# Optimization experiments

Measured on AMD Instinct MI355X. Metric: run time of the kernel, lower is better.

## Reference

```python
import jax, jax.numpy as jnp
import numpy as np

L, D_IN, D_HID, D_OUT, N = 8, 256, 1024, 256, 32768


def setup_inputs() -> dict:
    key = jax.random.key(0)
    kx, kp, kw1, kw2 = jax.random.split(key, 4)
    x = jax.random.normal(kx, (N, D_IN), dtype=jnp.float32)
    plane_idx = jax.random.randint(kp, (N,), 0, L, dtype=jnp.int32)
    W1 = jax.random.normal(kw1, (L, D_HID, D_IN), dtype=jnp.float32) * 0.014
    b1 = jnp.zeros((L, D_HID), dtype=jnp.float32)
    W2 = jax.random.normal(kw2, (L, D_OUT, D_HID), dtype=jnp.float32) * np.float32((2.0 / D_HID) ** 0.5)
    b2 = jnp.zeros((L, D_OUT), dtype=jnp.float32)
    return {"x": x, "W1": W1, "b1": b1, "W2": W2, "b2": b2, "plane_idx": plane_idx}


def reference(x, W1, b1, W2, b2, plane_idx):
    # Dense-dispatch MoE reference: scan over the L planes, run the full
    # 2-layer MLP for each plane's weights, and select per-walker rows via
    # the plane mask (equivalent math to gather -> MLP -> scatter).
    n_planes = W1.shape[0]
    out0 = jnp.zeros((x.shape[0], W2.shape[1]), dtype=x.dtype)

    def plane_step(out, p):
        h = jax.nn.gelu(x @ W1[p].T + b1[p], approximate=False)  # [N, D_hid]
        o = h @ W2[p].T + b2[p]                                  # [N, D_out]
        out = jnp.where((plane_idx == p)[:, None], o, out)
        return out, None

    out, _ = jax.lax.scan(plane_step, out0, jnp.arange(n_planes))
    return out
```

## Files before the change

### kernel.cpp

```cpp
#include <hip/hip_runtime.h>
#include <hip/hip_fp16.h>
#include <cstdint>

#define NT      32768
#define DIN     256
#define DHID    1024
#define DOUT    256
#define NPLANES 8
#define NBLK    (NT / 256)

typedef unsigned short u16;
typedef __attribute__((ext_vector_type(8))) _Float16 f16x8;
typedef __attribute__((ext_vector_type(4))) float    f32x4;

#define WS_OFFSETS 0
#define WS_META    64
#define WS_TP      1024
#define WS_TM      (WS_TP + 544*4)
#define WS_BLKHIST (WS_TM + 544*4)
#define WS_BLKBASE (WS_BLKHIST + NBLK*8*4)
#define WS_PERM    (WS_BLKBASE + NBLK*8*4)
#define WS_XB      (WS_PERM + NT*4)
#define WS_W1B     (WS_XB + NT*DIN*2)
#define WS_W2B     (WS_W1B + NPLANES*DHID*DIN*2)
#define WS_HB      (WS_W2B + NPLANES*DOUT*DHID*2)

__device__ __forceinline__ u16 f2h_bits(float f) {
    __half h = __float2half(f);
    return *reinterpret_cast<u16*>(&h);
}

__device__ __forceinline__ void gl_lds16(const void* g, void* l) {
    __builtin_amdgcn_global_load_lds(
        (const __attribute__((address_space(1))) void*)g,
        (__attribute__((address_space(3))) void*)l,
        16, 0, 0);
}

__global__ void prep_k(const int* __restrict__ pidx, const float* __restrict__ x,
                       const float* __restrict__ W1, const float* __restrict__ W2,
                       int* __restrict__ blkhist, u16* __restrict__ xb,
                       u16* __restrict__ w1b, u16* __restrict__ w2b) {
    __shared__ int cnt[NPLANES];
    const int t = threadIdx.x, lane = t & 63;
    if ((int)blockIdx.x < NBLK) {
        if (t < NPLANES) cnt[t] = 0;
        __syncthreads();
        const int p = pidx[blockIdx.x * 256 + t];
#pragma unroll
        for (int q = 0; q < NPLANES; ++q) {
            unsigned long long m = __ballot(p == q);
            if (p == q && __popcll(m & ((1ULL << lane) - 1)) == 0)
                atomicAdd(&cnt[q], __popcll(m));
        }
        __syncthreads();
        if (t < NPLANES) blkhist[blockIdx.x * NPLANES + t] = cnt[t];
    }
    const int n0 = NT * DIN / 4, n1 = NPLANES * DHID * DIN / 4, n2 = NPLANES * DOUT * DHID / 4;
    const int stride = gridDim.x * blockDim.x;
    for (int i = blockIdx.x * blockDim.x + t; i < n0 + n1 + n2; i += stride) {
        const float4* s; ushort4* d; int j;
        if (i < n0)           { s = (const float4*)x;  d = (ushort4*)xb;  j = i; }
        else if (i < n0 + n1) { s = (const float4*)W1; d = (ushort4*)w1b; j = i - n0; }
        else                  { s = (const float4*)W2; d = (ushort4*)w2b; j = i - n0 - n1; }
        float4 v = s[j];
        ushort4 o;
        o.x = f2h_bits(v.x); o.y = f2h_bits(v.y);
        o.z = f2h_bits(v.z); o.w = f2h_bits(v.w);
        d[j] = o;
    }
}

__global__ void scan_k(const int* __restrict__ blkhist, int* __restrict__ offsets,
                       int* __restrict__ blkbase, int* __restrict__ meta,
                       int* __restrict__ tp, int* __restrict__ tm) {
    __shared__ int tot[NPLANES];
    const int t = threadIdx.x;
    if (t < NPLANES) {
        int s = 0;
#pragma unroll 8
        for (int b = 0; b < NBLK; ++b) s += blkhist[b * NPLANES + t];
        tot[t] = s;
    }
    __syncthreads();
    if (t == 0) {
        int off = 0, tc = 0;
        for (int p = 0; p < NPLANES; ++p) {
            offsets[p] = off;
            for (int m = 0; m < tot[p]; m += 64) { tp[tc] = p; tm[tc] = m; ++tc; }
            off += tot[p];
        }
        offsets[NPLANES] = off;
        meta[0] = tc;
    }
    __syncthreads();
    if (t < NPLANES) {
        int run = offsets[t];
#pragma unroll 8
        for (int b = 0; b < NBLK; ++b) {
            blkbase[b * NPLANES + t] = run;
            run += blkhist[b * NPLANES + t];
        }
    }
}

__global__ void scatter_k(const int* __restrict__ pidx, const int* __restrict__ blkbase,
                          int* __restrict__ perm) {
    __shared__ int wcnt[4][NPLANES];
    __shared__ int wbase[4][NPLANES];
    const int t = threadIdx.x, lane = t & 63, wave = t >> 6;
    const int i = blockIdx.x * 256 + t;
    const int p = pidx[i];
    int rank = 0;
#pragma unroll
    for (int q = 0; q < NPLANES; ++q) {
        unsigned long long m = __ballot(p == q);
        if (lane == 0) wcnt[wave][q] = __popcll(m);
        if (p == q) rank = __popcll(m & ((1ULL << lane) - 1));
    }
    __syncthreads();
    if (t < NPLANES) {
        int run = blkbase[blockIdx.x * NPLANES + t];
#pragma unroll
        for (int w = 0; w < 4; ++w) { wbase[w][t] = run; run += wcnt[w][t]; }
    }
    __syncthreads();
    perm[wbase[wave][p] + rank] = i;
}

#define XCD_MAP(NSPLIT)                                                        \
    const int ntiles = meta[0];                                                \
    const int xcd = blockIdx.x & 7, idx = blockIdx.x >> 3;                     \
    const int q8 = ntiles >> 3, r8 = ntiles & 7;                               \
    const int tn = q8 + (xcd < r8 ? 1 : 0);                                    \
    if (idx >= tn * (NSPLIT)) return;                                          \
    const int tile = (xcd < r8 ? xcd * (q8 + 1)                                \
                               : r8 * (q8 + 1) + (xcd - r8) * q8)              \
                     + idx / (NSPLIT);                                         \
    const int n0v = (idx % (NSPLIT)) * 128;

__global__ __launch_bounds__(256, 4) void gemm1_k(
    const u16* __restrict__ xb, const u16* __restrict__ w1b,
    const float* __restrict__ b1, const int* __restrict__ perm,
    const int* __restrict__ offsets, const int* __restrict__ meta,
    const int* __restrict__ tp, const int* __restrict__ tm,
    u16* __restrict__ hb)
{
    __shared__ __align__(16) u16 smem[12288];
    XCD_MAP(8)
    const int p   = tp[tile];
    const int m0  = tm[tile];
    const int off = offsets[p];
    const int cnt = offsets[p + 1] - off;

    u16* const sA = smem;
    u16* const sB = smem + 4096;

    const int tid = threadIdx.x;
    const u16* aptr[2];
    const u16* bptr[4];
#pragma unroll
    for (int c = 0; c < 2; ++c) {
        const int slot = c * 256 + tid, row = slot >> 3, ch = slot & 7;
        const int gr = min(m0 + row, cnt - 1);
        aptr[c] = xb + (size_t)perm[off + gr] * DIN + ((ch ^ (row & 7)) * 8);
    }
#pragma unroll
    for (int c = 0; c < 4; ++c) {
        const int slot = c * 256 + tid, row = slot >> 3, ch = slot & 7;
        bptr[c] = w1b + ((size_t)p * DHID + n0v + row) * DIN + ((ch ^ (row & 7)) * 8);
    }
    const int wave = tid >> 6, lane = tid & 63;
    const int wr = wave >> 1, wc = wave & 1;
    const int lm = lane & 15, lk = lane >> 4;

    f32x4 acc[2][4];
#pragma unroll
    for (int a = 0; a < 2; ++a)
#pragma unroll
        for (int b = 0; b < 4; ++b) acc[a][b] = (f32x4){0.f, 0.f, 0.f, 0.f};

    for (int kt = 0; kt < DIN / 64; ++kt) {
        const int k0 = kt * 64;
#pragma unroll
        for (int c = 0; c < 2; ++c) gl_lds16(aptr[c] + k0, sA + c * 2048 + tid * 8);
#pragma unroll
        for (int c = 0; c < 4; ++c) gl_lds16(bptr[c] + k0, sB + c * 2048 + tid * 8);
        __syncthreads();
#pragma unroll
        for (int kk = 0; kk < 2; ++kk) {
            f16x8 af[2], bf[4];
#pragma unroll
            for (int mf = 0; mf < 2; ++mf) {
                const int row = wr * 32 + mf * 16 + lm;
                const int g   = kk * 4 + lk;
                af[mf] = *(const f16x8*)(sA + row * 64 + ((g ^ (row & 7)) * 8));
            }
#pragma unroll
            for (int nf = 0; nf < 4; ++nf) {
                const int row = wc * 64 + nf * 16 + lm;
                const int g   = kk * 4 + lk;
                bf[nf] = *(const f16x8*)(sB + row * 64 + ((g ^ (row & 7)) * 8));
            }
#pragma unroll
            for (int mf = 0; mf < 2; ++mf)
#pragma unroll
                for (int nf = 0; nf < 4; ++nf)
                    acc[mf][nf] = __builtin_amdgcn_mfma_f32_16x16x32_f16(
                        af[mf], bf[nf], acc[mf][nf], 0, 0, 0);
        }
        __syncthreads();
    }

    u16* const sOut = smem;
#pragma unroll
    for (int nf = 0; nf < 4; ++nf) {
        const int col = wc * 64 + nf * 16 + lm;
        const float bb = b1[p * DHID + n0v + col];
        const int cc = col >> 3, c7 = col & 7;
#pragma unroll
        for (int mf = 0; mf < 2; ++mf) {
#pragma unroll
            for (int j = 0; j < 4; ++j) {
                const int tok = wr * 32 + mf * 16 + lk * 4 + j;
                float v = acc[mf][nf][j] + bb;
                float g = 0.5f * v * (1.0f + erff(v * 0.70710678118654752f));
                sOut[tok * 128 + ((cc ^ (tok & 15)) * 8) + c7] = f2h_bits(g);
            }
        }
    }
    __syncthreads();
    const int r = tid >> 2, qq = tid & 3;
    if (m0 + r < cnt) {
        u16* dst = hb + (size_t)(off + m0 + r) * DHID + n0v;
#pragma unroll
        for (int c = 0; c < 4; ++c) {
            const int l = qq * 4 + c;
            *(int4*)(dst + l * 8) = *(const int4*)(sOut + r * 128 + ((l ^ (r & 15)) * 8));
        }
    }
}

__global__ __launch_bounds__(256, 4) void gemm2_k(
    const u16* __restrict__ hb, const u16* __restrict__ w2b,
    const float* __restrict__ b2, const int* __restrict__ perm,
    const int* __restrict__ offsets, const int* __restrict__ meta,
    const int* __restrict__ tp, const int* __restrict__ tm,
    float* __restrict__ out)
{
    __shared__ __align__(16) u16 smem[12288];
    XCD_MAP(2)
    const int p   = tp[tile];
    const int m0  = tm[tile];
    const int off = offsets[p];
    const int cnt = offsets[p + 1] - off;

    u16* const sA = smem;
    u16* const sB = smem + 4096;

    const int tid = threadIdx.x;
    const u16* aptr[2];
    const u16* bptr[4];
#pragma unroll
    for (int c = 0; c < 2; ++c) {
        const int slot = c * 256 + tid, row = slot >> 3, ch = slot & 7;
        aptr[c] = hb + (size_t)(off + min(m0 + row, cnt - 1)) * DHID + ((ch ^ (row & 7)) * 8);
    }
#pragma unroll
    for (int c = 0; c < 4; ++c) {
        const int slot = c * 256 + tid, row = slot >> 3, ch = slot & 7;
        bptr[c] = w2b + ((size_t)p * DOUT + n0v + row) * DHID + ((ch ^ (row & 7)) * 8);
    }
    const int wave = tid >> 6, lane = tid & 63;
    const int wr = wave >> 1, wc = wave & 1;
    const int lm = lane & 15, lk = lane >> 4;

    f32x4 acc[2][4];
#pragma unroll
    for (int a = 0; a < 2; ++a)
#pragma unroll
        for (int b = 0; b < 4; ++b) acc[a][b] = (f32x4){0.f, 0.f, 0.f, 0.f};

    for (int kt = 0; kt < DHID / 64; ++kt) {
        const int k0 = kt * 64;
#pragma unroll
        for (int c = 0; c < 2; ++c) gl_lds16(aptr[c] + k0, sA + c * 2048 + tid * 8);
#pragma unroll
        for (int c = 0; c < 4; ++c) gl_lds16(bptr[c] + k0, sB + c * 2048 + tid * 8);
        __syncthreads();
#pragma unroll
        for (int kk = 0; kk < 2; ++kk) {
            f16x8 af[2], bf[4];
#pragma unroll
            for (int mf = 0; mf < 2; ++mf) {
                const int row = wr * 32 + mf * 16 + lm;
                const int g   = kk * 4 + lk;
                af[mf] = *(const f16x8*)(sA + row * 64 + ((g ^ (row & 7)) * 8));
            }
#pragma unroll
            for (int nf = 0; nf < 4; ++nf) {
                const int row = wc * 64 + nf * 16 + lm;
                const int g   = kk * 4 + lk;
                bf[nf] = *(const f16x8*)(sB + row * 64 + ((g ^ (row & 7)) * 8));
            }
#pragma unroll
            for (int mf = 0; mf < 2; ++mf)
#pragma unroll
                for (int nf = 0; nf < 4; ++nf)
                    acc[mf][nf] = __builtin_amdgcn_mfma_f32_16x16x32_f16(
                        af[mf], bf[nf], acc[mf][nf], 0, 0, 0);
        }
        __syncthreads();
    }

#pragma unroll
    for (int nf = 0; nf < 4; ++nf) {
        const int col = n0v + wc * 64 + nf * 16 + lm;
        const float bb = b2[p * DOUT + col];
#pragma unroll
        for (int mf = 0; mf < 2; ++mf) {
#pragma unroll
            for (int j = 0; j < 4; ++j) {
                const int tok = wr * 32 + mf * 16 + lk * 4 + j;
                if (m0 + tok < cnt)
                    out[(size_t)perm[off + m0 + tok] * DOUT + col] = acc[mf][nf][j] + bb;
            }
        }
    }
}

extern "C" void kernel_launch(void* const* d_in, const int* in_sizes, int n_in,
                              void* d_out, int out_size, void* d_ws, size_t ws_size,
                              hipStream_t stream) {
    const float* x    = (const float*)d_in[0];
    const float* W1   = (const float*)d_in[1];
    const float* b1   = (const float*)d_in[2];
    const float* W2   = (const float*)d_in[3];
    const float* b2   = (const float*)d_in[4];
    const int*   pidx = (const int*)d_in[5];
    float*       out  = (float*)d_out;

    char* ws      = (char*)d_ws;
    int* offsets  = (int*)(ws + WS_OFFSETS);
    int* meta     = (int*)(ws + WS_META);
    int* tp       = (int*)(ws + WS_TP);
    int* tm       = (int*)(ws + WS_TM);
    int* blkhist  = (int*)(ws + WS_BLKHIST);
    int* blkbase  = (int*)(ws + WS_BLKBASE);
    int* perm     = (int*)(ws + WS_PERM);
    u16* xb       = (u16*)(ws + WS_XB);
    u16* w1b      = (u16*)(ws + WS_W1B);
    u16* w2b      = (u16*)(ws + WS_W2B);
    u16* hb       = (u16*)(ws + WS_HB);

    prep_k<<<2048, 256, 0, stream>>>(pidx, x, W1, W2, blkhist, xb, w1b, w2b);
    scan_k<<<1, 64, 0, stream>>>(blkhist, offsets, blkbase, meta, tp, tm);
    scatter_k<<<NBLK, 256, 0, stream>>>(pidx, blkbase, perm);

    gemm1_k<<<4224, 256, 0, stream>>>(xb, w1b, b1, perm, offsets, meta, tp, tm, hb);
    gemm2_k<<<1056, 256, 0, stream>>>(hb, w2b, b2, perm, offsets, meta, tp, tm, out);
}
```

Measured before the change: 115.5 us.

## Enlarge gemm1 token tile to 128 rows and use sigmoid-form GELU approximation

gemm1 now processes 128-token tiles with 512 threads, so each loaded W1 slice is reused across twice as many tokens. The scan kernel builds separate tile lists for gemm1 (128-row) and gemm2 (64-row), and the launch grids change to match. The exact erf GELU is replaced with a tanh-style approximation computed as x*sigmoid, using a fast exp and a reciprocal, to cut the cost of the epilogue. The approximation adds a small numerical deviation from the exact GELU. The aggressive launch bounds may also limit registers per thread and cause spills.

```diff
diff --git a/kernel.cpp b/kernel.cpp
--- a/kernel.cpp
+++ b/kernel.cpp
@@ -15,9 +15,11 @@
 
 #define WS_OFFSETS 0
 #define WS_META    64
-#define WS_TP      1024
-#define WS_TM      (WS_TP + 544*4)
-#define WS_BLKHIST (WS_TM + 544*4)
+#define WS_T1P     1024
+#define WS_T1M     (WS_T1P + 272*4)
+#define WS_T2P     (WS_T1M + 272*4)
+#define WS_T2M     (WS_T2P + 544*4)
+#define WS_BLKHIST (WS_T2M + 544*4)
 #define WS_BLKBASE (WS_BLKHIST + NBLK*8*4)
 #define WS_PERM    (WS_BLKBASE + NBLK*8*4)
 #define WS_XB      (WS_PERM + NT*4)
@@ -35,6 +37,12 @@
         (const __attribute__((address_space(1))) void*)g,
         (__attribute__((address_space(3))) void*)l,
         16, 0, 0);
+}
+
+__device__ __forceinline__ float gelu_fast(float x) {
+    const float u = x * (1.5957691216f + 0.07135481283f * x * x);
+    const float e = __expf(-u);
+    return x * __builtin_amdgcn_rcpf(1.0f + e);
 }
 
 __global__ void prep_k(const int* __restrict__ pidx, const float* __restrict__ x,
@@ -73,7 +81,8 @@
 
 __global__ void scan_k(const int* __restrict__ blkhist, int* __restrict__ offsets,
                        int* __restrict__ blkbase, int* __restrict__ meta,
-                       int* __restrict__ tp, int* __restrict__ tm) {
+                       int* __restrict__ t1p, int* __restrict__ t1m,
+                       int* __restrict__ t2p, int* __restrict__ t2m) {
     __shared__ int tot[NPLANES];
     const int t = threadIdx.x;
     if (t < NPLANES) {
@@ -84,14 +93,15 @@
     }
     __syncthreads();
     if (t == 0) {
-        int off = 0, tc = 0;
+        int off = 0, tc1 = 0, tc2 = 0;
         for (int p = 0; p < NPLANES; ++p) {
             offsets[p] = off;
-            for (int m = 0; m < tot[p]; m += 64) { tp[tc] = p; tm[tc] = m; ++tc; }
+            for (int m = 0; m < tot[p]; m += 128) { t1p[tc1] = p; t1m[tc1] = m; ++tc1; }
+            for (int m = 0; m < tot[p]; m += 64)  { t2p[tc2] = p; t2m[tc2] = m; ++tc2; }
             off += tot[p];
         }
         offsets[NPLANES] = off;
-        meta[0] = tc;
+        meta[0] = tc1; meta[1] = tc2;
     }
     __syncthreads();
     if (t < NPLANES) {
@@ -128,8 +138,8 @@
     perm[wbase[wave][p] + rank] = i;
 }
 
-#define XCD_MAP(NSPLIT)                                                        \
-    const int ntiles = meta[0];                                                \
+#define XCD_MAP(NSPLIT, NTILES)                                                \
+    const int ntiles = (NTILES);                                               \
     const int xcd = blockIdx.x & 7, idx = blockIdx.x >> 3;                     \
     const int q8 = ntiles >> 3, r8 = ntiles & 7;                               \
     const int tn = q8 + (xcd < r8 ? 1 : 0);                                    \
@@ -139,35 +149,31 @@
                      + idx / (NSPLIT);                                         \
     const int n0v = (idx % (NSPLIT)) * 128;
 
-__global__ __launch_bounds__(256, 4) void gemm1_k(
+__global__ __launch_bounds__(512, 8) void gemm1_k(
     const u16* __restrict__ xb, const u16* __restrict__ w1b,
     const float* __restrict__ b1, const int* __restrict__ perm,
     const int* __restrict__ offsets, const int* __restrict__ meta,
     const int* __restrict__ tp, const int* __restrict__ tm,
     u16* __restrict__ hb)
 {
-    __shared__ __align__(16) u16 smem[12288];
-    XCD_MAP(8)
+    __shared__ __align__(16) u16 smem[16384];
+    XCD_MAP(8, meta[0])
     const int p   = tp[tile];
     const int m0  = tm[tile];
     const int off = offsets[p];
     const int cnt = offsets[p + 1] - off;
 
     u16* const sA = smem;
-    u16* const sB = smem + 4096;
+    u16* const sB = smem + 8192;
 
     const int tid = threadIdx.x;
     const u16* aptr[2];
-    const u16* bptr[4];
+    const u16* bptr[2];
 #pragma unroll
     for (int c = 0; c < 2; ++c) {
-        const int slot = c * 256 + tid, row = slot >> 3, ch = slot & 7;
+        const int slot = c * 512 + tid, row = slot >> 3, ch = slot & 7;
         const int gr = min(m0 + row, cnt - 1);
         aptr[c] = xb + (size_t)perm[off + gr] * DIN + ((ch ^ (row & 7)) * 8);
-    }
-#pragma unroll
-    for (int c = 0; c < 4; ++c) {
-        const int slot = c * 256 + tid, row = slot >> 3, ch = slot & 7;
         bptr[c] = w1b + ((size_t)p * DHID + n0v + row) * DIN + ((ch ^ (row & 7)) * 8);
     }
     const int wave = tid >> 6, lane = tid & 63;
@@ -183,9 +189,10 @@
     for (int kt = 0; kt < DIN / 64; ++kt) {
         const int k0 = kt * 64;
 #pragma unroll
-        for (int c = 0; c < 2; ++c) gl_lds16(aptr[c] + k0, sA + c * 2048 + tid * 8);
-#pragma unroll
-        for (int c = 0; c < 4; ++c) gl_lds16(bptr[c] + k0, sB + c * 2048 + tid * 8);
+        for (int c = 0; c < 2; ++c) {
+            gl_lds16(aptr[c] + k0, sA + c * 4096 + tid * 8);
+            gl_lds16(bptr[c] + k0, sB + c * 4096 + tid * 8);
+        }
         __syncthreads();
 #pragma unroll
         for (int kk = 0; kk < 2; ++kk) {
@@ -223,9 +230,8 @@
 #pragma unroll
             for (int j = 0; j < 4; ++j) {
                 const int tok = wr * 32 + mf * 16 + lk * 4 + j;
-                float v = acc[mf][nf][j] + bb;
-                float g = 0.5f * v * (1.0f + erff(v * 0.70710678118654752f));
-                sOut[tok * 128 + ((cc ^ (tok & 15)) * 8) + c7] = f2h_bits(g);
+                sOut[tok * 128 + ((cc ^ (tok & 15)) * 8) + c7] =
+                    f2h_bits(gelu_fast(acc[mf][nf][j] + bb));
             }
         }
     }
@@ -249,7 +255,7 @@
     float* __restrict__ out)
 {
     __shared__ __align__(16) u16 smem[12288];
-    XCD_MAP(2)
+    XCD_MAP(2, meta[1])
     const int p   = tp[tile];
     const int m0  = tm[tile];
     const int off = offsets[p];
@@ -343,8 +349,10 @@
     char* ws      = (char*)d_ws;
     int* offsets  = (int*)(ws + WS_OFFSETS);
     int* meta     = (int*)(ws + WS_META);
-    int* tp       = (int*)(ws + WS_TP);
-    int* tm       = (int*)(ws + WS_TM);
+    int* t1p      = (int*)(ws + WS_T1P);
+    int* t1m      = (int*)(ws + WS_T1M);
+    int* t2p      = (int*)(ws + WS_T2P);
+    int* t2m      = (int*)(ws + WS_T2M);
     int* blkhist  = (int*)(ws + WS_BLKHIST);
     int* blkbase  = (int*)(ws + WS_BLKBASE);
     int* perm     = (int*)(ws + WS_PERM);
@@ -354,9 +362,9 @@
     u16* hb       = (u16*)(ws + WS_HB);
 
     prep_k<<<2048, 256, 0, stream>>>(pidx, x, W1, W2, blkhist, xb, w1b, w2b);
-    scan_k<<<1, 64, 0, stream>>>(blkhist, offsets, blkbase, meta, tp, tm);
+    scan_k<<<1, 64, 0, stream>>>(blkhist, offsets, blkbase, meta, t1p, t1m, t2p, t2m);
     scatter_k<<<NBLK, 256, 0, stream>>>(pidx, blkbase, perm);
 
-    gemm1_k<<<4224, 256, 0, stream>>>(xb, w1b, b1, perm, offsets, meta, tp, tm, hb);
-    gemm2_k<<<1056, 256, 0, stream>>>(hb, w2b, b2, perm, offsets, meta, tp, tm, out);
-}
+    gemm1_k<<<2176, 512, 0, stream>>>(xb, w1b, b1, perm, offsets, meta, t1p, t1m, hb);
+    gemm2_k<<<1104, 256, 0, stream>>>(hb, w2b, b2, perm, offsets, meta, t2p, t2m, out);
+}
```

Measured after the change: 145.4 us. +25.8%, slower.

## Widen gemm1 tiles to 64x256 and replace erf GELU with fast sigmoid approximation

Applied to the files above, without the earlier changes.

Gemm1 now computes a 64-token by 256-hidden tile per block instead of 64x128, with each wave owning a 64-column strip and all four M fragments. This halves the number of gemm1 blocks and cuts the redundant gathered-activation loads per hidden column, at the cost of more LDS per block and more accumulator registers. The exact erf GELU is replaced by a tanh-style approximation built on exp and a reciprocal, which lowers epilogue cost but changes numerics slightly. Grid sizes for both GEMMs are also adjusted.

```diff
diff --git a/kernel.cpp b/kernel.cpp
--- a/kernel.cpp
+++ b/kernel.cpp
@@ -35,6 +35,12 @@
         (const __attribute__((address_space(1))) void*)g,
         (__attribute__((address_space(3))) void*)l,
         16, 0, 0);
+}
+
+__device__ __forceinline__ float gelu_fast(float x) {
+    const float u = x * (1.5957691216f + 0.07135481283f * x * x);
+    const float e = __expf(-u);
+    return x * __builtin_amdgcn_rcpf(1.0f + e);
 }
 
 __global__ void prep_k(const int* __restrict__ pidx, const float* __restrict__ x,
@@ -128,7 +134,7 @@
     perm[wbase[wave][p] + rank] = i;
 }
 
-#define XCD_MAP(NSPLIT)                                                        \
+#define XCD_MAP(NSPLIT, NW)                                                    \
     const int ntiles = meta[0];                                                \
     const int xcd = blockIdx.x & 7, idx = blockIdx.x >> 3;                     \
     const int q8 = ntiles >> 3, r8 = ntiles & 7;                               \
@@ -137,7 +143,7 @@
     const int tile = (xcd < r8 ? xcd * (q8 + 1)                                \
                                : r8 * (q8 + 1) + (xcd - r8) * q8)              \
                      + idx / (NSPLIT);                                         \
-    const int n0v = (idx % (NSPLIT)) * 128;
+    const int n0v = (idx % (NSPLIT)) * (NW);
 
 __global__ __launch_bounds__(256, 4) void gemm1_k(
     const u16* __restrict__ xb, const u16* __restrict__ w1b,
@@ -146,8 +152,8 @@
     const int* __restrict__ tp, const int* __restrict__ tm,
     u16* __restrict__ hb)
 {
-    __shared__ __align__(16) u16 smem[12288];
-    XCD_MAP(8)
+    __shared__ __align__(16) u16 smem[20480];
+    XCD_MAP(4, 256)
     const int p   = tp[tile];
     const int m0  = tm[tile];
     const int off = offsets[p];
@@ -156,27 +162,27 @@
     u16* const sA = smem;
     u16* const sB = smem + 4096;
 
-    const int tid = threadIdx.x;
+    const int tid = threadIdx.x, srow = tid >> 3, sch = tid & 7;
     const u16* aptr[2];
-    const u16* bptr[4];
 #pragma unroll
     for (int c = 0; c < 2; ++c) {
-        const int slot = c * 256 + tid, row = slot >> 3, ch = slot & 7;
-        const int gr = min(m0 + row, cnt - 1);
-        aptr[c] = xb + (size_t)perm[off + gr] * DIN + ((ch ^ (row & 7)) * 8);
-    }
-#pragma unroll
-    for (int c = 0; c < 4; ++c) {
-        const int slot = c * 256 + tid, row = slot >> 3, ch = slot & 7;
-        bptr[c] = w1b + ((size_t)p * DHID + n0v + row) * DIN + ((ch ^ (row & 7)) * 8);
+        const int row = c * 32 + srow;
+        const int gr  = min(m0 + row, cnt - 1);
+        aptr[c] = xb + (size_t)perm[off + gr] * DIN + ((sch ^ (srow & 7)) * 8);
+    }
+    const u16* bptr[8];
+#pragma unroll
+    for (int c = 0; c < 8; ++c) {
+        const int row = c * 32 + srow;
+        bptr[c] = w1b + ((size_t)p * DHID + n0v + row) * DIN + ((sch ^ (srow & 7)) * 8);
     }
     const int wave = tid >> 6, lane = tid & 63;
-    const int wr = wave >> 1, wc = wave & 1;
+    const int wc = wave;
     const int lm = lane & 15, lk = lane >> 4;
 
-    f32x4 acc[2][4];
-#pragma unroll
-    for (int a = 0; a < 2; ++a)
+    f32x4 acc[4][4];
+#pragma unroll
+    for (int a = 0; a < 4; ++a)
 #pragma unroll
         for (int b = 0; b < 4; ++b) acc[a][b] = (f32x4){0.f, 0.f, 0.f, 0.f};
 
@@ -185,29 +191,26 @@
 #pragma unroll
         for (int c = 0; c < 2; ++c) gl_lds16(aptr[c] + k0, sA + c * 2048 + tid * 8);
 #pragma unroll
-        for (int c = 0; c < 4; ++c) gl_lds16(bptr[c] + k0, sB + c * 2048 + tid * 8);
+        for (int c = 0; c < 8; ++c) gl_lds16(bptr[c] + k0, sB + c * 2048 + tid * 8);
         __syncthreads();
 #pragma unroll
         for (int kk = 0; kk < 2; ++kk) {
-            f16x8 af[2], bf[4];
-#pragma unroll
-            for (int mf = 0; mf < 2; ++mf) {
-                const int row = wr * 32 + mf * 16 + lm;
-                const int g   = kk * 4 + lk;
+            const int g = kk * 4 + lk;
+            f16x8 af[4];
+#pragma unroll
+            for (int mf = 0; mf < 4; ++mf) {
+                const int row = mf * 16 + lm;
                 af[mf] = *(const f16x8*)(sA + row * 64 + ((g ^ (row & 7)) * 8));
             }
 #pragma unroll
             for (int nf = 0; nf < 4; ++nf) {
                 const int row = wc * 64 + nf * 16 + lm;
-                const int g   = kk * 4 + lk;
-                bf[nf] = *(const f16x8*)(sB + row * 64 + ((g ^ (row & 7)) * 8));
-            }
-#pragma unroll
-            for (int mf = 0; mf < 2; ++mf)
-#pragma unroll
-                for (int nf = 0; nf < 4; ++nf)
+                const f16x8 bf = *(const f16x8*)(sB + row * 64 + ((g ^ (row & 7)) * 8));
+#pragma unroll
+                for (int mf = 0; mf < 4; ++mf)
                     acc[mf][nf] = __builtin_amdgcn_mfma_f32_16x16x32_f16(
-                        af[mf], bf[nf], acc[mf][nf], 0, 0, 0);
+                        af[mf], bf, acc[mf][nf], 0, 0, 0);
+            }
         }
         __syncthreads();
     }
@@ -219,13 +222,12 @@
         const float bb = b1[p * DHID + n0v + col];
         const int cc = col >> 3, c7 = col & 7;
 #pragma unroll
-        for (int mf = 0; mf < 2; ++mf) {
+        for (int mf = 0; mf < 4; ++mf) {
 #pragma unroll
             for (int j = 0; j < 4; ++j) {
-                const int tok = wr * 32 + mf * 16 + lk * 4 + j;
-                float v = acc[mf][nf][j] + bb;
-                float g = 0.5f * v * (1.0f + erff(v * 0.70710678118654752f));
-                sOut[tok * 128 + ((cc ^ (tok & 15)) * 8) + c7] = f2h_bits(g);
+                const int tok = mf * 16 + lk * 4 + j;
+                sOut[tok * 256 + ((cc ^ (tok & 31)) * 8) + c7] =
+                    f2h_bits(gelu_fast(acc[mf][nf][j] + bb));
             }
         }
     }
@@ -234,9 +236,9 @@
     if (m0 + r < cnt) {
         u16* dst = hb + (size_t)(off + m0 + r) * DHID + n0v;
 #pragma unroll
-        for (int c = 0; c < 4; ++c) {
-            const int l = qq * 4 + c;
-            *(int4*)(dst + l * 8) = *(const int4*)(sOut + r * 128 + ((l ^ (r & 15)) * 8));
+        for (int c = 0; c < 8; ++c) {
+            const int l = qq * 8 + c;
+            *(int4*)(dst + l * 8) = *(const int4*)(sOut + r * 256 + ((l ^ (r & 31)) * 8));
         }
     }
 }
@@ -249,7 +251,7 @@
     float* __restrict__ out)
 {
     __shared__ __align__(16) u16 smem[12288];
-    XCD_MAP(2)
+    XCD_MAP(2, 128)
     const int p   = tp[tile];
     const int m0  = tm[tile];
     const int off = offsets[p];
@@ -357,6 +359,6 @@
     scan_k<<<1, 64, 0, stream>>>(blkhist, offsets, blkbase, meta, tp, tm);
     scatter_k<<<NBLK, 256, 0, stream>>>(pidx, blkbase, perm);
 
-    gemm1_k<<<4224, 256, 0, stream>>>(xb, w1b, b1, perm, offsets, meta, tp, tm, hb);
-    gemm2_k<<<1056, 256, 0, stream>>>(hb, w2b, b2, perm, offsets, meta, tp, tm, out);
-}
+    gemm1_k<<<2080, 256, 0, stream>>>(xb, w1b, b1, perm, offsets, meta, tp, tm, hb);
+    gemm2_k<<<1040, 256, 0, stream>>>(hb, w2b, b2, perm, offsets, meta, tp, tm, out);
+}
```

New measurement: 117.7 us. Within noise of the previous version (+1.8%).
